# Performance work log

Measured on AMD Instinct MI355X. Metric: run time of the kernel, lower is better.

The kernel has to match this reference:

```python
import jax, jax.numpy as jnp
import numpy as np

ROPE_DIM = 64
GN_GROUPS = 8
GN_CH = 512
GN_EPS = 1e-6


def rope_rotate(t, rot_dim=ROPE_DIM, offset=0):
    # lucidrains-style rotary embedding on first rot_dim features, interleaved pairs
    n = t.shape[-2]
    inv_freq = 1.0 / (10000.0 ** (jnp.arange(0, rot_dim, 2, dtype=jnp.float32) / rot_dim))
    pos = jnp.arange(n, dtype=jnp.float32) + offset
    freqs = pos[:, None] * inv_freq[None, :]           # (n, rot_dim//2)
    freqs = jnp.repeat(freqs, 2, axis=-1)              # (n, rot_dim)
    cos, sin = jnp.cos(freqs), jnp.sin(freqs)
    t_rot, t_pass = t[..., :rot_dim], t[..., rot_dim:]
    x = t_rot.reshape(t_rot.shape[:-1] + (rot_dim // 2, 2))
    rot_half = jnp.stack((-x[..., 1], x[..., 0]), axis=-1).reshape(t_rot.shape)
    return jnp.concatenate([t_rot * cos + rot_half * sin, t_pass], axis=-1)


def group_norm_rows(x, w, b, groups=GN_GROUPS, eps=GN_EPS):
    # GroupNorm applied to x reshaped as (-1, C): each row is a sample
    shp = x.shape
    r = x.reshape(-1, groups, GN_CH // groups)
    mu = r.mean(axis=-1, keepdims=True)
    var = r.var(axis=-1, keepdims=True)
    r = (r - mu) * jax.lax.rsqrt(var + eps)
    return (r.reshape(-1, GN_CH) * w + b).reshape(shp)


def setup_inputs() -> dict:
    key = jax.random.key(0)
    ks = jax.random.split(key, 8)
    B, S, D = 4, 8192, 512
    s = 1.0 / np.sqrt(D)
    return {
        "X_Q": jax.random.normal(ks[0], (B, S, D), jnp.float32),
        "X_KV": jax.random.normal(ks[1], (B, S, D), jnp.float32),
        "S_h": jnp.zeros((1,), jnp.float32),
        "S_C": jnp.zeros((1,), jnp.float32),
        "Wq": jax.random.normal(ks[2], (D, D), jnp.float32) * s,
        "bq": jnp.zeros((D,), jnp.float32),
        "Wk": jax.random.normal(ks[3], (D, D), jnp.float32) * s,
        "bk": jnp.zeros((D,), jnp.float32),
        "Wv": jax.random.normal(ks[4], (D, D), jnp.float32) * s,
        "bv": jnp.zeros((D,), jnp.float32),
        "gn_w": jnp.ones((GN_CH,), jnp.float32),
        "gn_b": jnp.zeros((GN_CH,), jnp.float32),
    }


def reference(X_Q, X_KV, S_h, S_C, Wq, bq, Wk, bk, Wv, bv, gn_w, gn_b):
    Q = X_Q @ Wq.T + bq
    V = X_KV @ Wv.T + bv
    # NOTE: faithful to source: K = rope(V), the proj_K output is rotated-V
    _K_unused = X_KV @ Wk.T + bk
    Q = rope_rotate(Q)
    K = rope_rotate(V)
    Q = jax.nn.silu(Q)
    K = jax.nn.silu(K)
    V = jax.nn.silu(V)
    # (Q @ K^T)^T @ V == K @ (Q^T @ V): linear-attention rewrite, O(n*d^2)
    QtV = jnp.einsum('bnd,bne->bde', Q, V)
    out = jnp.einsum('bnd,bde->bne', K, QtV)
    # dropout is identity in eval mode (p=0)
    out = group_norm_rows(out, gn_w, gn_b)
    return (out, S_h, S_C)
```

## Files before the change

### kernel.cpp

```cpp
#include <hip/hip_runtime.h>

typedef __bf16 bf16x8 __attribute__((ext_vector_type(8)));
typedef float f32x4 __attribute__((ext_vector_type(4)));
typedef unsigned short u16x8 __attribute__((ext_vector_type(8)));
typedef unsigned short u16x4 __attribute__((ext_vector_type(4)));

__device__ __forceinline__ unsigned short f2b_u(float f) {
  unsigned int u;
  __builtin_memcpy(&u, &f, 4);
  unsigned int r = 0x7FFFu + ((u >> 16) & 1u);
  return (unsigned short)((u + r) >> 16);
}
__device__ __forceinline__ float silu_f(float x) { return x / (1.f + expf(-x)); }

__global__ __launch_bounds__(256) void cvt_w(const float* __restrict__ in,
                                             unsigned short* __restrict__ out) {
  int i = (blockIdx.x * 256 + threadIdx.x) * 4;
  f32x4 x = *(const f32x4*)(in + i);
  u16x4 o;
#pragma unroll
  for (int j = 0; j < 4; ++j) o[j] = f2b_u(x[j]);
  *(u16x4*)(out + i) = o;
}

__global__ __launch_bounds__(256) void gen_tbl(float* __restrict__ T) {
  int idx = blockIdx.x * 256 + threadIdx.x;
  int pos = idx >> 5, ip = idx & 31;
  float f = (float)pos * powf(10000.f, -(float)ip * (1.f / 32.f));
  float sn, cs;
  sincosf(f, &sn, &cs);
  T[idx * 2] = sn;
  T[idx * 2 + 1] = cs;
}

template <int MODE>
__global__ __launch_bounds__(1024) void proj2(
    const float* __restrict__ A, const unsigned short* __restrict__ B,
    unsigned short* __restrict__ Ct, const float* __restrict__ bias,
    unsigned short* __restrict__ Cn, const float* __restrict__ TBL) {
  __shared__ __align__(16) unsigned short smem[25600];
  unsigned short(*sA)[40] = (unsigned short(*)[40])smem;
  unsigned short(*sB)[40] = (unsigned short(*)[40])(smem + 5120);
  unsigned short* sT = smem;

  const int m0 = blockIdx.x << 7;
  const int tid = threadIdx.x;
  const int lane = tid & 63, w = tid >> 6;
  const int wm = (w & 1) << 6, wn = (w >> 1) << 6;
  const int l16 = lane & 15, q8 = (lane >> 4) << 3;
  const int ar = tid >> 3, ac = (tid & 7) << 2;
  const int br = tid >> 1, bc = (tid & 1) << 4;

  f32x4 acc[4][4] = {};

  for (int kt = 0; kt < 512; kt += 32) {
    f32x4 av = *(const f32x4*)(A + (long)(m0 + ar) * 512 + kt + ac);
    u16x8 b0 = *(const u16x8*)(B + (long)br * 512 + kt + bc);
    u16x8 b1 = *(const u16x8*)(B + (long)br * 512 + kt + bc + 8);
    u16x4 a4;
#pragma unroll
    for (int j = 0; j < 4; ++j) a4[j] = f2b_u(av[j]);
    __syncthreads();
    *(u16x4*)&sA[ar][ac] = a4;
    *(u16x8*)&sB[br][bc] = b0;
    *(u16x8*)&sB[br][bc + 8] = b1;
    __syncthreads();
    bf16x8 af[4], bf[4];
#pragma unroll
    for (int i = 0; i < 4; ++i) af[i] = *(const bf16x8*)&sA[wm + (i << 4) + l16][q8];
#pragma unroll
    for (int j = 0; j < 4; ++j) bf[j] = *(const bf16x8*)&sB[wn + (j << 4) + l16][q8];
#pragma unroll
    for (int i = 0; i < 4; ++i)
#pragma unroll
      for (int j = 0; j < 4; ++j)
        acc[i][j] = __builtin_amdgcn_mfma_f32_16x16x32_bf16(af[i], bf[j], acc[i][j], 0, 0, 0);
  }

  const int rq = (lane >> 4) << 2;
#pragma unroll
  for (int j = 0; j < 4; ++j) {
    float bv = bias[wn + (j << 4) + l16];
#pragma unroll
    for (int i = 0; i < 4; ++i)
#pragma unroll
      for (int r = 0; r < 4; ++r) acc[i][j][r] += bv;
  }
  const int bq_ = m0 >> 13;
  const int s0_ = m0 & 8191;

  if (MODE == 0 && wn == 0) {
#pragma unroll
    for (int j = 0; j < 4; ++j) {
      int ip = (j << 3) + (l16 >> 1);
      float sgn = (l16 & 1) ? 1.f : -1.f;
#pragma unroll
      for (int i = 0; i < 4; ++i)
#pragma unroll
        for (int r = 0; r < 4; ++r) {
          int pos = s0_ + wm + (i << 4) + rq + r;
          const float* t = TBL + ((long)pos << 6) + (ip << 1);
          float sn = t[0], cs = t[1];
          float v = acc[i][j][r];
          float p = __shfl_xor(v, 1);
          acc[i][j][r] = v * cs + sgn * sn * p;
        }
    }
  }

  unsigned short* dstT = Ct + ((long)bq_ << 22);
#pragma unroll
  for (int p = 0; p < 4; ++p) {
    __syncthreads();
    if ((w & 1) == (p >> 1)) {
      int ib = (p & 1) << 1;
#pragma unroll
      for (int ii = 0; ii < 2; ++ii) {
#pragma unroll
        for (int j = 0; j < 4; ++j)
#pragma unroll
          for (int r = 0; r < 4; ++r)
            sT[(wn + (j << 4) + l16) * 40 + (ii << 4) + rq + r] =
                f2b_u(silu_f(acc[ib + ii][j][r]));
      }
    }
    __syncthreads();
    int row = tid >> 1, cb = (tid & 1) << 4;
    u16x8 v0 = *(const u16x8*)&sT[row * 40 + cb];
    u16x8 v1 = *(const u16x8*)&sT[row * 40 + cb + 8];
    long o = (long)row * 8192 + s0_ + (p << 5) + cb;
    *(u16x8*)(dstT + o) = v0;
    *(u16x8*)(dstT + o + 8) = v1;
  }

  if (MODE == 1) {
    if (wn == 0) {
#pragma unroll
      for (int j = 0; j < 4; ++j) {
        int ip = (j << 3) + (l16 >> 1);
        float sgn = (l16 & 1) ? 1.f : -1.f;
#pragma unroll
        for (int i = 0; i < 4; ++i)
#pragma unroll
          for (int r = 0; r < 4; ++r) {
            int pos = s0_ + wm + (i << 4) + rq + r;
            const float* t = TBL + ((long)pos << 6) + (ip << 1);
            float sn = t[0], cs = t[1];
            float v = acc[i][j][r];
            float p = __shfl_xor(v, 1);
            acc[i][j][r] = v * cs + sgn * sn * p;
          }
      }
    }
#pragma unroll
    for (int p = 0; p < 4; ++p) {
      __syncthreads();
      if ((w & 1) == (p >> 1)) {
        int ib = (p & 1) << 1;
#pragma unroll
        for (int ii = 0; ii < 2; ++ii) {
#pragma unroll
          for (int j = 0; j < 4; ++j)
#pragma unroll
            for (int r = 0; r < 4; ++r)
              sT[((ii << 4) + rq + r) * 520 + wn + (j << 4) + l16] =
                  f2b_u(silu_f(acc[ib + ii][j][r]));
        }
      }
      __syncthreads();
      int row = tid >> 5, cb = (tid & 31) << 4;
      u16x8 v0 = *(const u16x8*)&sT[row * 520 + cb];
      u16x8 v1 = *(const u16x8*)&sT[row * 520 + cb + 8];
      long o = (long)(m0 + (p << 5) + row) * 512 + cb;
      *(u16x8*)(Cn + o) = v0;
      *(u16x8*)(Cn + o + 8) = v1;
    }
  }
}

__global__ __launch_bounds__(256) void gemm_qtv(
    const unsigned short* __restrict__ A, const unsigned short* __restrict__ B,
    float* __restrict__ Cp) {
  __shared__ __align__(16) unsigned short smem[18432];
  unsigned short(*sA)[72] = (unsigned short(*)[72])smem;
  unsigned short(*sB)[72] = (unsigned short(*)[72])(smem + 9216);

  const int blk = blockIdx.x;
  const int low3 = blk & 7, hi = blk >> 3;
  const int m = ((low3 & 1) << 1) | (hi & 1);
  const int n = (low3 & 2) | ((hi >> 1) & 1);
  const int z = ((hi >> 2) << 1) | (low3 >> 2);
  const int batch = z >> 3, kc = z & 7;
  const unsigned short* A0 = A + (long)batch * 4194304 + (long)kc * 1024;
  const unsigned short* B0 = B + (long)batch * 4194304 + (long)kc * 1024;
  const int m0 = m << 7, n0 = n << 7;
  const int tid = threadIdx.x;
  const int lane = tid & 63, wave = tid >> 6;
  const int wm = (wave & 1) << 6, wn = (wave >> 1) << 6;
  const int l16 = lane & 15, q8 = (lane >> 4) << 3;

  f32x4 acc[4][4] = {};

  for (int kt = 0; kt < 1024; kt += 64) {
    u16x8 ra[4], rb[4];
#pragma unroll
    for (int i = 0; i < 4; ++i) {
      int c = tid + (i << 8);
      int row = c >> 3, col = (c & 7) << 3;
      ra[i] = *(const u16x8*)(A0 + (long)(m0 + row) * 8192 + kt + col);
      rb[i] = *(const u16x8*)(B0 + (long)(n0 + row) * 8192 + kt + col);
    }
    __syncthreads();
#pragma unroll
    for (int i = 0; i < 4; ++i) {
      int c = tid + (i << 8);
      int row = c >> 3, col = (c & 7) << 3;
      *(u16x8*)&sA[row][col] = ra[i];
      *(u16x8*)&sB[row][col] = rb[i];
    }
    __syncthreads();
#pragma unroll
    for (int kk = 0; kk < 2; ++kk) {
      bf16x8 af[4], bfv[4];
#pragma unroll
      for (int i = 0; i < 4; ++i) {
        af[i] = *(const bf16x8*)&sA[wm + (i << 4) + l16][(kk << 5) + q8];
        bfv[i] = *(const bf16x8*)&sB[wn + (i << 4) + l16][(kk << 5) + q8];
      }
#pragma unroll
      for (int i = 0; i < 4; ++i)
#pragma unroll
        for (int j = 0; j < 4; ++j)
          acc[i][j] = __builtin_amdgcn_mfma_f32_16x16x32_bf16(af[i], bfv[j], acc[i][j], 0, 0, 0);
    }
  }

  const int rq = (lane >> 4) << 2;
#pragma unroll
  for (int i = 0; i < 4; ++i)
#pragma unroll
    for (int j = 0; j < 4; ++j)
#pragma unroll
      for (int r = 0; r < 4; ++r) {
        int gm = m0 + wm + (i << 4) + rq + r;
        int gn = n0 + wn + (j << 4) + l16;
        atomicAdd(Cp + (long)batch * 262144 + (long)gm * 512 + gn, acc[i][j][r]);
      }
}

__global__ __launch_bounds__(64) void colmean(const float* __restrict__ C, float* __restrict__ Cd) {
  const int bd = blockIdx.x;
  const int b = bd >> 9, d = bd & 511;
  const float* p = C + ((long)b << 18) + d;
  float s = 0.f;
  for (int e = threadIdx.x; e < 512; e += 64) s += p[(long)e << 9];
  s += __shfl_xor(s, 1);
  s += __shfl_xor(s, 2);
  s += __shfl_xor(s, 4);
  s += __shfl_xor(s, 8);
  s += __shfl_xor(s, 16);
  s += __shfl_xor(s, 32);
  if (threadIdx.x == 0) Cd[bd] = s * (1.f / 512.f);
}

__global__ __launch_bounds__(256) void cvt_center(const float* __restrict__ in,
                                                  const float* __restrict__ Cd,
                                                  unsigned short* __restrict__ out,
                                                  const float* __restrict__ Sh,
                                                  const float* __restrict__ Sc,
                                                  float* __restrict__ outp) {
  int i = (blockIdx.x * 256 + threadIdx.x) * 4;
  f32x4 x = *(const f32x4*)(in + i);
  int b = i >> 18, d = i & 511;
  f32x4 c = *(const f32x4*)(Cd + (b << 9) + d);
  u16x4 o;
#pragma unroll
  for (int j = 0; j < 4; ++j) o[j] = f2b_u(x[j] - c[j]);
  *(u16x4*)(out + i) = o;
  if (blockIdx.x == 0 && threadIdx.x == 0) {
    outp[16777216] = Sh[0];
    outp[16777217] = Sc[0];
  }
}

__global__ __launch_bounds__(256) void gemm4_gn(
    const unsigned short* __restrict__ A, const unsigned short* __restrict__ B,
    const float* __restrict__ gnw, const float* __restrict__ gnb,
    float* __restrict__ out) {
  __shared__ __align__(16) unsigned short smem[18432];
  unsigned short(*sA)[72] = (unsigned short(*)[72])smem;
  unsigned short(*sB)[72] = (unsigned short(*)[72])(smem + 9216);

  const int blk = blockIdx.x;
  const int mt = blk & 255, n = blk >> 8;
  const int batch = mt >> 6;
  const int m0 = (mt & 63) << 7, n0 = n << 7;
  const unsigned short* A0 = A + (long)batch * 4194304;
  const unsigned short* B0 = B + (long)batch * 262144;
  const int tid = threadIdx.x;
  const int lane = tid & 63, wave = tid >> 6;
  const int wm = (wave & 1) << 6, wn = (wave >> 1) << 6;
  const int l16 = lane & 15, q8 = (lane >> 4) << 3;

  f32x4 acc[4][4] = {};

  for (int kt = 0; kt < 512; kt += 64) {
    u16x8 ra[4], rb[4];
#pragma unroll
    for (int i = 0; i < 4; ++i) {
      int c = tid + (i << 8);
      int row = c >> 3, col = (c & 7) << 3;
      ra[i] = *(const u16x8*)(A0 + (long)(m0 + row) * 512 + kt + col);
      rb[i] = *(const u16x8*)(B0 + (long)(n0 + row) * 512 + kt + col);
    }
    __syncthreads();
#pragma unroll
    for (int i = 0; i < 4; ++i) {
      int c = tid + (i << 8);
      int row = c >> 3, col = (c & 7) << 3;
      *(u16x8*)&sA[row][col] = ra[i];
      *(u16x8*)&sB[row][col] = rb[i];
    }
    __syncthreads();
#pragma unroll
    for (int kk = 0; kk < 2; ++kk) {
      bf16x8 af[4], bfv[4];
#pragma unroll
      for (int i = 0; i < 4; ++i) {
        af[i] = *(const bf16x8*)&sA[wm + (i << 4) + l16][(kk << 5) + q8];
        bfv[i] = *(const bf16x8*)&sB[wn + (i << 4) + l16][(kk << 5) + q8];
      }
#pragma unroll
      for (int i = 0; i < 4; ++i)
#pragma unroll
        for (int j = 0; j < 4; ++j)
          acc[i][j] = __builtin_amdgcn_mfma_f32_16x16x32_bf16(af[i], bfv[j], acc[i][j], 0, 0, 0);
    }
  }

  const int rq = (lane >> 4) << 2;
  float wv[4], bb[4];
#pragma unroll
  for (int j = 0; j < 4; ++j) {
    int gn = n0 + wn + (j << 4) + l16;
    wv[j] = gnw[gn];
    bb[j] = gnb[gn];
  }
  float* obase = out + (long)batch * 4194304;
#pragma unroll
  for (int i = 0; i < 4; ++i) {
    float mean[4], inv[4];
#pragma unroll
    for (int r = 0; r < 4; ++r) {
      float s = acc[i][0][r] + acc[i][1][r] + acc[i][2][r] + acc[i][3][r];
      s += __shfl_xor(s, 1);
      s += __shfl_xor(s, 2);
      s += __shfl_xor(s, 4);
      s += __shfl_xor(s, 8);
      mean[r] = s * (1.f / 64.f);
      float sq = 0.f;
#pragma unroll
      for (int j = 0; j < 4; ++j) {
        float d = acc[i][j][r] - mean[r];
        sq += d * d;
      }
      sq += __shfl_xor(sq, 1);
      sq += __shfl_xor(sq, 2);
      sq += __shfl_xor(sq, 4);
      sq += __shfl_xor(sq, 8);
      inv[r] = rsqrtf(sq * (1.f / 64.f) + 1e-6f);
    }
#pragma unroll
    for (int j = 0; j < 4; ++j) {
      int gn = n0 + wn + (j << 4) + l16;
#pragma unroll
      for (int r = 0; r < 4; ++r) {
        int gm = m0 + wm + (i << 4) + rq + r;
        obase[(long)gm * 512 + gn] = (acc[i][j][r] - mean[r]) * inv[r] * wv[j] + bb[j];
      }
    }
  }
}

extern "C" void kernel_launch(void* const* d_in, const int* in_sizes, int n_in,
                              void* d_out, int out_size, void* d_ws, size_t ws_size,
                              hipStream_t stream) {
  const float* Xq = (const float*)d_in[0];
  const float* Xkv = (const float*)d_in[1];
  const float* Sh = (const float*)d_in[2];
  const float* Sc = (const float*)d_in[3];
  const float* Wq = (const float*)d_in[4];
  const float* bq = (const float*)d_in[5];
  const float* Wv = (const float*)d_in[8];
  const float* bv = (const float*)d_in[9];
  const float* gnw = (const float*)d_in[10];
  const float* gnb = (const float*)d_in[11];

  char* ws = (char*)d_ws;
  unsigned short* QT = (unsigned short*)(ws);
  unsigned short* VT = (unsigned short*)(ws + 33554432L);
  unsigned short* Kn = (unsigned short*)(ws + 67108864L);
  float* C2f = (float*)(ws + 100663296L);
  unsigned short* C2c = (unsigned short*)(ws + 104857600L);
  float* Cd = (float*)(ws + 106954752L);
  unsigned short* Wqb = (unsigned short*)(ws + 100663296L);
  unsigned short* Wvb = (unsigned short*)(ws + 100663296L + 524288L);
  float* TBL = (float*)(ws + 100663296L + 1048576L);
  float* outp = (float*)d_out;

  if (ws_size < 106962944UL) return;

  cvt_w<<<256, 256, 0, stream>>>(Wq, Wqb);
  cvt_w<<<256, 256, 0, stream>>>(Wv, Wvb);
  gen_tbl<<<1024, 256, 0, stream>>>(TBL);

  proj2<0><<<256, 1024, 0, stream>>>(Xq, Wqb, QT, bq, nullptr, TBL);
  proj2<1><<<256, 1024, 0, stream>>>(Xkv, Wvb, VT, bv, Kn, TBL);

  (void)hipMemsetAsync(C2f, 0, 4194304, stream);
  gemm_qtv<<<512, 256, 0, stream>>>(VT, QT, C2f);

  colmean<<<2048, 64, 0, stream>>>(C2f, Cd);
  cvt_center<<<1024, 256, 0, stream>>>(C2f, Cd, C2c, Sh, Sc, outp);

  gemm4_gn<<<1024, 256, 0, stream>>>(Kn, C2c, gnw, gnb, outp);
}
```

Measured before the change: 404.4 us.

## Retile projection GEMM into 64x256 blocks with register prefetch and dual-layout MFMA output

Replaces the 128x512 projection tile (1024 threads, 256 blocks) with 64x256 tiles (512 threads, 1024 blocks), adding register prefetch of the next K-slice so global loads overlap the MFMAs. For the KV projection, a second MFMA pass with swapped operands produces the row-major K output directly in registers, replacing the LDS transpose staging and its extra barriers. Outputs are now written straight from registers as 8-byte stores. In exchange it doubles MFMA work in MODE 1, re-reads the X rows for each of the two N halves, and uses narrower, less coalesced global stores.

Result: faster. 383.5 us (-5.2%).

```diff
diff --git a/kernel.cpp b/kernel.cpp
--- a/kernel.cpp
+++ b/kernel.cpp
@@ -34,116 +34,92 @@
 }
 
 template <int MODE>
-__global__ __launch_bounds__(1024) void proj2(
+__global__ __launch_bounds__(512, 4) void proj4(
     const float* __restrict__ A, const unsigned short* __restrict__ B,
     unsigned short* __restrict__ Ct, const float* __restrict__ bias,
     unsigned short* __restrict__ Cn, const float* __restrict__ TBL) {
-  __shared__ __align__(16) unsigned short smem[25600];
-  unsigned short(*sA)[40] = (unsigned short(*)[40])smem;
-  unsigned short(*sB)[40] = (unsigned short(*)[40])(smem + 5120);
-  unsigned short* sT = smem;
-
-  const int m0 = blockIdx.x << 7;
+  __shared__ __align__(16) unsigned short sA[64][40];
+  __shared__ __align__(16) unsigned short sB[256][40];
+
+  const int bid = blockIdx.x;
+  const int n0 = (bid & 1) << 8;
+  const long m0 = (long)(bid >> 1) << 6;
   const int tid = threadIdx.x;
   const int lane = tid & 63, w = tid >> 6;
-  const int wm = (w & 1) << 6, wn = (w >> 1) << 6;
-  const int l16 = lane & 15, q8 = (lane >> 4) << 3;
+  const int wn = w << 5;
+  const int l16 = lane & 15, q8 = (lane >> 4) << 3, rq = (lane >> 4) << 2;
   const int ar = tid >> 3, ac = (tid & 7) << 2;
   const int br = tid >> 1, bc = (tid & 1) << 4;
 
-  f32x4 acc[4][4] = {};
+  const float* Ap = A + (m0 + ar) * 512 + ac;
+  const unsigned short* Bp = B + (long)(n0 + br) * 512 + bc;
+
+  f32x4 acc[4][2] = {};
+  f32x4 acc2[2][4] = {};
+
+  f32x4 av = *(const f32x4*)Ap;
+  u16x8 b0 = *(const u16x8*)Bp;
+  u16x8 b1 = *(const u16x8*)(Bp + 8);
 
   for (int kt = 0; kt < 512; kt += 32) {
-    f32x4 av = *(const f32x4*)(A + (long)(m0 + ar) * 512 + kt + ac);
-    u16x8 b0 = *(const u16x8*)(B + (long)br * 512 + kt + bc);
-    u16x8 b1 = *(const u16x8*)(B + (long)br * 512 + kt + bc + 8);
-    u16x4 a4;
-#pragma unroll
-    for (int j = 0; j < 4; ++j) a4[j] = f2b_u(av[j]);
-    __syncthreads();
-    *(u16x4*)&sA[ar][ac] = a4;
-    *(u16x8*)&sB[br][bc] = b0;
-    *(u16x8*)&sB[br][bc + 8] = b1;
-    __syncthreads();
-    bf16x8 af[4], bf[4];
-#pragma unroll
-    for (int i = 0; i < 4; ++i) af[i] = *(const bf16x8*)&sA[wm + (i << 4) + l16][q8];
-#pragma unroll
-    for (int j = 0; j < 4; ++j) bf[j] = *(const bf16x8*)&sB[wn + (j << 4) + l16][q8];
+    __syncthreads();
+    {
+      u16x4 a4;
+#pragma unroll
+      for (int j = 0; j < 4; ++j) a4[j] = f2b_u(av[j]);
+      *(u16x4*)&sA[ar][ac] = a4;
+      *(u16x8*)&sB[br][bc] = b0;
+      *(u16x8*)&sB[br][bc + 8] = b1;
+    }
+    __syncthreads();
+    if (kt < 480) {
+      av = *(const f32x4*)(Ap + kt + 32);
+      b0 = *(const u16x8*)(Bp + kt + 32);
+      b1 = *(const u16x8*)(Bp + kt + 40);
+    }
+    bf16x8 af[4], bf[2];
+#pragma unroll
+    for (int i = 0; i < 4; ++i) af[i] = *(const bf16x8*)&sA[(i << 4) + l16][q8];
+#pragma unroll
+    for (int j = 0; j < 2; ++j) bf[j] = *(const bf16x8*)&sB[wn + (j << 4) + l16][q8];
 #pragma unroll
     for (int i = 0; i < 4; ++i)
 #pragma unroll
-      for (int j = 0; j < 4; ++j)
+      for (int j = 0; j < 2; ++j)
         acc[i][j] = __builtin_amdgcn_mfma_f32_16x16x32_bf16(af[i], bf[j], acc[i][j], 0, 0, 0);
-  }
-
-  const int rq = (lane >> 4) << 2;
-#pragma unroll
-  for (int j = 0; j < 4; ++j) {
-    float bv = bias[wn + (j << 4) + l16];
+    if (MODE == 1) {
+#pragma unroll
+      for (int ci = 0; ci < 2; ++ci)
+#pragma unroll
+        for (int sj = 0; sj < 4; ++sj)
+          acc2[ci][sj] =
+              __builtin_amdgcn_mfma_f32_16x16x32_bf16(bf[ci], af[sj], acc2[ci][sj], 0, 0, 0);
+    }
+  }
+
+  const int batch = (int)(m0 >> 13);
+  const int s0 = ((int)m0) & 8191;
+
+#pragma unroll
+  for (int j = 0; j < 2; ++j) {
+    float bv = bias[n0 + wn + (j << 4) + l16];
 #pragma unroll
     for (int i = 0; i < 4; ++i)
 #pragma unroll
       for (int r = 0; r < 4; ++r) acc[i][j][r] += bv;
   }
-  const int bq_ = m0 >> 13;
-  const int s0_ = m0 & 8191;
-
-  if (MODE == 0 && wn == 0) {
-#pragma unroll
-    for (int j = 0; j < 4; ++j) {
-      int ip = (j << 3) + (l16 >> 1);
-      float sgn = (l16 & 1) ? 1.f : -1.f;
-#pragma unroll
-      for (int i = 0; i < 4; ++i)
-#pragma unroll
-        for (int r = 0; r < 4; ++r) {
-          int pos = s0_ + wm + (i << 4) + rq + r;
-          const float* t = TBL + ((long)pos << 6) + (ip << 1);
-          float sn = t[0], cs = t[1];
-          float v = acc[i][j][r];
-          float p = __shfl_xor(v, 1);
-          acc[i][j][r] = v * cs + sgn * sn * p;
-        }
-    }
-  }
-
-  unsigned short* dstT = Ct + ((long)bq_ << 22);
-#pragma unroll
-  for (int p = 0; p < 4; ++p) {
-    __syncthreads();
-    if ((w & 1) == (p >> 1)) {
-      int ib = (p & 1) << 1;
-#pragma unroll
-      for (int ii = 0; ii < 2; ++ii) {
-#pragma unroll
-        for (int j = 0; j < 4; ++j)
-#pragma unroll
-          for (int r = 0; r < 4; ++r)
-            sT[(wn + (j << 4) + l16) * 40 + (ii << 4) + rq + r] =
-                f2b_u(silu_f(acc[ib + ii][j][r]));
-      }
-    }
-    __syncthreads();
-    int row = tid >> 1, cb = (tid & 1) << 4;
-    u16x8 v0 = *(const u16x8*)&sT[row * 40 + cb];
-    u16x8 v1 = *(const u16x8*)&sT[row * 40 + cb + 8];
-    long o = (long)row * 8192 + s0_ + (p << 5) + cb;
-    *(u16x8*)(dstT + o) = v0;
-    *(u16x8*)(dstT + o + 8) = v1;
-  }
-
-  if (MODE == 1) {
-    if (wn == 0) {
-#pragma unroll
-      for (int j = 0; j < 4; ++j) {
-        int ip = (j << 3) + (l16 >> 1);
+
+  if (MODE == 0) {
+    if (n0 + wn < 64) {
+#pragma unroll
+      for (int j = 0; j < 2; ++j) {
+        int ip = ((wn + (j << 4)) >> 1) + (l16 >> 1);
         float sgn = (l16 & 1) ? 1.f : -1.f;
 #pragma unroll
         for (int i = 0; i < 4; ++i)
 #pragma unroll
           for (int r = 0; r < 4; ++r) {
-            int pos = s0_ + wm + (i << 4) + rq + r;
+            int pos = s0 + (i << 4) + rq + r;
             const float* t = TBL + ((long)pos << 6) + (ip << 1);
             float sn = t[0], cs = t[1];
             float v = acc[i][j][r];
@@ -152,29 +128,60 @@
           }
       }
     }
-#pragma unroll
-    for (int p = 0; p < 4; ++p) {
-      __syncthreads();
-      if ((w & 1) == (p >> 1)) {
-        int ib = (p & 1) << 1;
-#pragma unroll
-        for (int ii = 0; ii < 2; ++ii) {
-#pragma unroll
-          for (int j = 0; j < 4; ++j)
-#pragma unroll
-            for (int r = 0; r < 4; ++r)
-              sT[((ii << 4) + rq + r) * 520 + wn + (j << 4) + l16] =
-                  f2b_u(silu_f(acc[ib + ii][j][r]));
+  }
+
+  {
+    unsigned short* dstT = Ct + ((long)batch << 22);
+#pragma unroll
+    for (int i = 0; i < 4; ++i)
+#pragma unroll
+      for (int j = 0; j < 2; ++j) {
+        u16x4 o;
+#pragma unroll
+        for (int r = 0; r < 4; ++r) o[r] = f2b_u(silu_f(acc[i][j][r]));
+        *(u16x4*)(dstT + (long)(n0 + wn + (j << 4) + l16) * 8192 + s0 + (i << 4) + rq) = o;
+      }
+  }
+
+  if (MODE == 1) {
+#pragma unroll
+    for (int ci = 0; ci < 2; ++ci) {
+      float bv2[4];
+#pragma unroll
+      for (int r = 0; r < 4; ++r) bv2[r] = bias[n0 + wn + (ci << 4) + rq + r];
+#pragma unroll
+      for (int sj = 0; sj < 4; ++sj)
+#pragma unroll
+        for (int r = 0; r < 4; ++r) acc2[ci][sj][r] += bv2[r];
+    }
+    if (n0 + wn < 64) {
+#pragma unroll
+      for (int ci = 0; ci < 2; ++ci)
+#pragma unroll
+        for (int sj = 0; sj < 4; ++sj) {
+          int pos = s0 + (sj << 4) + l16;
+          const float* tb = TBL + ((long)pos << 6);
+#pragma unroll
+          for (int rp = 0; rp < 4; rp += 2) {
+            int ip = (wn + (ci << 4) + rq + rp) >> 1;
+            float sn = tb[ip << 1], cs = tb[(ip << 1) + 1];
+            float v0 = acc2[ci][sj][rp], v1 = acc2[ci][sj][rp + 1];
+            acc2[ci][sj][rp] = v0 * cs - sn * v1;
+            acc2[ci][sj][rp + 1] = v1 * cs + sn * v0;
+          }
         }
-      }
-      __syncthreads();
-      int row = tid >> 5, cb = (tid & 31) << 4;
-      u16x8 v0 = *(const u16x8*)&sT[row * 520 + cb];
-      u16x8 v1 = *(const u16x8*)&sT[row * 520 + cb + 8];
-      long o = (long)(m0 + (p << 5) + row) * 512 + cb;
-      *(u16x8*)(Cn + o) = v0;
-      *(u16x8*)(Cn + o + 8) = v1;
-    }
+    }
+    unsigned short* dstN = Cn + ((long)batch << 22);
+#pragma unroll
+    for (int ci = 0; ci < 2; ++ci)
+#pragma unroll
+      for (int sj = 0; sj < 4; ++sj) {
+        u16x4 o;
+#pragma unroll
+        for (int r = 0; r < 4; ++r) o[r] = f2b_u(silu_f(acc2[ci][sj][r]));
+        int seq = s0 + (sj << 4) + l16;
+        *(u16x4*)(dstN + (long)seq * 512 + n0 + wn + (ci << 4) + rq) = o;
+      }
   }
 }
 
@@ -414,8 +421,8 @@
   cvt_w<<<256, 256, 0, stream>>>(Wv, Wvb);
   gen_tbl<<<1024, 256, 0, stream>>>(TBL);
 
-  proj2<0><<<256, 1024, 0, stream>>>(Xq, Wqb, QT, bq, nullptr, TBL);
-  proj2<1><<<256, 1024, 0, stream>>>(Xkv, Wvb, VT, bv, Kn, TBL);
+  proj4<0><<<1024, 512, 0, stream>>>(Xq, Wqb, QT, bq, nullptr, TBL);
+  proj4<1><<<1024, 512, 0, stream>>>(Xkv, Wvb, VT, bv, Kn, TBL);
 
   (void)hipMemsetAsync(C2f, 0, 4194304, stream);
   gemm_qtv<<<512, 256, 0, stream>>>(VT, QT, C2f);
```
